# Optimization experiments

Hardware: AMD Instinct MI355X
Metric: run time of the kernel (lower is better)

## Reference

```python
import jax, jax.numpy as jnp
import numpy as np

HEAD_DIM = 64
D_MODEL = 512
B, T = 8, 2048


def setup_inputs() -> dict:
    key = jax.random.key(0)
    kx, kk, kq, kv = jax.random.split(key, 4)
    x = jax.random.normal(kx, (B, T, D_MODEL), dtype=jnp.float32)
    s = 1.0 / np.sqrt(D_MODEL)
    # torch nn.Linear weights are [out, in]
    Wk = jax.random.uniform(kk, (HEAD_DIM, D_MODEL), jnp.float32, -s, s)
    Wq = jax.random.uniform(kq, (HEAD_DIM, D_MODEL), jnp.float32, -s, s)
    Wv = jax.random.uniform(kv, (HEAD_DIM, D_MODEL), jnp.float32, -s, s)
    mask = jnp.ones((1,), dtype=bool)  # not-None sentinel -> causal masking on
    return {"x": x, "Wk": Wk, "Wq": Wq, "Wv": Wv, "mask": mask}


def reference(x, Wk, Wq, Wv, mask):
    Bc, Tc, C = x.shape
    k = jnp.einsum("btc,hc->bth", x, Wk)
    q = jnp.einsum("btc,hc->bth", x, Wq)
    v = jnp.einsum("btc,hc->bth", x, Wv)
    # NOTE: source scales by C**-0.5 where C == d_model (not head_dim)
    scores = jnp.einsum("bih,bjh->bij", q, k) * (C ** -0.5)  # [B,T,T]
    causal = jnp.tril(jnp.ones((Tc, Tc), dtype=bool))
    scores = jnp.where(causal[None, :, :], scores, -jnp.inf)
    # NOTE: source applies softmax over dim=1 (query axis), faithfully kept
    attn_weights = jax.nn.softmax(scores, axis=1)
    output = jnp.einsum("bij,bjh->bih", attn_weights, v)  # [B,T,head_dim]
    return (output, attn_weights)
```

## Files before the change

kernel.cpp:

```cpp
#include <hip/hip_runtime.h>
#include <hip/hip_bf16.h>

#define TT 2048
#define NB 8
#define DM 512
#define HD 64
static constexpr float SCALE = 0.04419417382415922f;

typedef short  s16x8 __attribute__((ext_vector_type(8)));
typedef float  f32x4 __attribute__((ext_vector_type(4)));

#define MFMA(a, b, c) __builtin_amdgcn_mfma_f32_16x16x32_bf16((a), (b), (c), 0, 0, 0)

static __device__ inline unsigned short f2bf(float f) {
    unsigned int u = __float_as_uint(f);
    u += 0x7FFFu + ((u >> 16) & 1u);
    return (unsigned short)(u >> 16);
}

__global__ __launch_bounds__(256) void prep_kernel(
    const float* __restrict__ Wk, const float* __restrict__ Wq,
    const float* __restrict__ Wv, unsigned short* __restrict__ wbf,
    float* __restrict__ colsum, float* __restrict__ out) {
    const int bi = blockIdx.x, t = threadIdx.x;
    if (bi < 256) {
        int i = (bi * 256 + t) * 4;
        *(float4*)(out + i) = make_float4(0.f, 0.f, 0.f, 0.f);
    } else if (bi < 260) {
        int i = ((bi - 256) * 256 + t) * 4;
        *(float4*)(colsum + i) = make_float4(0.f, 0.f, 0.f, 0.f);
    } else {
        int g = ((bi - 260) * 256 + t) * 4;
        int mat = g >> 15, off = g & 32767;
        const float* src = (mat == 0) ? Wk : (mat == 1) ? Wq : Wv;
        float4 f = *(const float4*)(src + off);
        wbf[g + 0] = f2bf(f.x); wbf[g + 1] = f2bf(f.y);
        wbf[g + 2] = f2bf(f.z); wbf[g + 3] = f2bf(f.w);
    }
}

__global__ __launch_bounds__(256) void rcp_kernel(float* __restrict__ p) {
    int i = (blockIdx.x * 256 + threadIdx.x) * 4;
    float4 a = *(float4*)(p + i);
    a.x = 1.0f / a.x; a.y = 1.0f / a.y; a.z = 1.0f / a.z; a.w = 1.0f / a.w;
    *(float4*)(p + i) = a;
}

#define XS 72
__global__ __launch_bounds__(256) void qkv_kernel(
    const float* __restrict__ x, const unsigned short* __restrict__ wbf,
    unsigned short* __restrict__ kb, unsigned short* __restrict__ qb,
    unsigned short* __restrict__ vb) {
    __shared__ unsigned short xs[32 * XS];
    const int i0 = blockIdx.x * 32;
    const int t = threadIdx.x;
    const int w = t >> 6, lane = t & 63;
    const int m15 = lane & 15, quad = lane >> 4;
    const int srow = t >> 3, c8 = (t & 7) * 8;
    f32x4 acc[2][3];
    for (int mt = 0; mt < 2; ++mt)
        for (int ct = 0; ct < 3; ++ct)
            acc[mt][ct] = (f32x4){0.f, 0.f, 0.f, 0.f};

    for (int kc = 0; kc < DM; kc += 64) {
        __syncthreads();
        {
            const float* gp = x + (size_t)(i0 + srow) * DM + kc + c8;
            float4 f0 = *(const float4*)gp;
            float4 f1 = *(const float4*)(gp + 4);
            s16x8 h;
            h[0] = (short)f2bf(f0.x); h[1] = (short)f2bf(f0.y);
            h[2] = (short)f2bf(f0.z); h[3] = (short)f2bf(f0.w);
            h[4] = (short)f2bf(f1.x); h[5] = (short)f2bf(f1.y);
            h[6] = (short)f2bf(f1.z); h[7] = (short)f2bf(f1.w);
            *(s16x8*)(xs + srow * XS + c8) = h;
        }
        __syncthreads();
        for (int ks = 0; ks < 2; ++ks) {
            s16x8 a[2];
            for (int mt = 0; mt < 2; ++mt)
                a[mt] = *(const s16x8*)(xs + (mt * 16 + m15) * XS + ks * 32 + quad * 8);
            for (int ct = 0; ct < 3; ++ct) {
                s16x8 bfr = *(const s16x8*)(wbf +
                    (size_t)((w * 3 + ct) * 16 + m15) * DM + kc + ks * 32 + quad * 8);
                acc[0][ct] = MFMA(a[0], bfr, acc[0][ct]);
                acc[1][ct] = MFMA(a[1], bfr, acc[1][ct]);
            }
        }
    }
    for (int mt = 0; mt < 2; ++mt)
        for (int ct = 0; ct < 3; ++ct) {
            int tile16 = w * 3 + ct;
            unsigned short* outp = (tile16 < 4) ? kb : (tile16 < 8) ? qb : vb;
            int col = (tile16 & 3) * 16 + m15;
            for (int r = 0; r < 4; ++r) {
                int grow = i0 + mt * 16 + quad * 4 + r;
                outp[(size_t)grow * HD + col] = f2bf(acc[mt][ct][r]);
            }
        }
}

__global__ __launch_bounds__(256) void colsum_kernel(
    const unsigned short* __restrict__ qb, const unsigned short* __restrict__ kb,
    float* __restrict__ colsum) {
    const int jt = blockIdx.x, ich = blockIdx.y, b = blockIdx.z;
    const int j0 = jt * 64;
    const int iend = (ich + 1) * 512;
    if (iend <= j0) return;
    const int t = threadIdx.x;
    const int w = t >> 6, lane = t & 63;
    const int m15 = lane & 15, quad = lane >> 4;
    s16x8 bk[4][2];
    for (int ct = 0; ct < 4; ++ct)
        for (int ks = 0; ks < 2; ++ks)
            bk[ct][ks] = *(const s16x8*)(kb +
                (size_t)(b * TT + j0 + ct * 16 + m15) * HD + ks * 32 + quad * 8);
    float csum[4] = {0.f, 0.f, 0.f, 0.f};
    const int istart = max(ich * 512, j0);
    for (int it = istart + w * 16; it < iend; it += 64) {
        s16x8 aq[2];
        for (int ks = 0; ks < 2; ++ks)
            aq[ks] = *(const s16x8*)(qb +
                (size_t)(b * TT + it + m15) * HD + ks * 32 + quad * 8);
        for (int ct = 0; ct < 4; ++ct) {
            f32x4 s = (f32x4){0.f, 0.f, 0.f, 0.f};
            s = MFMA(aq[0], bk[ct][0], s);
            s = MFMA(aq[1], bk[ct][1], s);
            int gj = j0 + ct * 16 + m15;
            for (int r = 0; r < 4; ++r) {
                int gi = it + quad * 4 + r;
                float e = (gj <= gi) ? __expf(s[r] * SCALE) : 0.f;
                csum[ct] += e;
            }
        }
    }
    for (int ct = 0; ct < 4; ++ct) {
        csum[ct] += __shfl_xor(csum[ct], 16);
        csum[ct] += __shfl_xor(csum[ct], 32);
    }
    if (lane < 16)
        for (int ct = 0; ct < 4; ++ct)
            atomicAdd(&colsum[b * TT + j0 + ct * 16 + lane], csum[ct]);
}

#define VS 264
#define PS 72
__global__ __launch_bounds__(256) void normpv_kernel(
    const unsigned short* __restrict__ qb, const unsigned short* __restrict__ kb,
    const unsigned short* __restrict__ vb, const float* __restrict__ rcs,
    float* __restrict__ attn, float* __restrict__ out) {
    const int jch = blockIdx.x;
    const int ti = blockIdx.y, b = blockIdx.z;
    const int i0 = ti * 64;
    const int jbase = jch * 512;
    float* abase = attn + (size_t)b * TT * TT;
    const int t = threadIdx.x;
    const float4 z = make_float4(0.f, 0.f, 0.f, 0.f);
    if (jbase > i0 + 63) {
        for (int e = 0; e < 32; ++e) {
            int f4 = e * 256 + t;
            int row = f4 >> 7, c4 = (f4 & 127) * 4;
            *(float4*)(abase + (size_t)(i0 + row) * TT + jbase + c4) = z;
        }
        return;
    }
    const int w = t >> 6, lane = t & 63;
    const int m15 = lane & 15, quad = lane >> 4;
    __shared__ unsigned short vT[64 * VS];
    __shared__ unsigned short ps[4 * 16 * PS];
    unsigned short* psw = ps + w * 16 * PS;
    s16x8 aq[2];
    for (int ks = 0; ks < 2; ++ks)
        aq[ks] = *(const s16x8*)(qb +
            (size_t)(b * TT + i0 + w * 16 + m15) * HD + ks * 32 + quad * 8);
    f32x4 o[4];
    for (int ht = 0; ht < 4; ++ht) o[ht] = (f32x4){0.f, 0.f, 0.f, 0.f};
    const float* rcb = rcs + b * TT;

    for (int half = 0; half < 2; ++half) {
        const int jh = jbase + half * 256;
        if (jh > i0 + 63) {
            for (int e = 0; e < 16; ++e) {
                int f4 = e * 256 + t;
                int row = f4 >> 6, c4 = (f4 & 63) * 4;
                *(float4*)(abase + (size_t)(i0 + row) * TT + jh + c4) = z;
            }
            continue;
        }
        __syncthreads();
        {
            const unsigned short* vp = vb + (size_t)(b * TT + jh + t) * HD;
            for (int seg = 0; seg < 8; ++seg) {
                s16x8 vv = *(const s16x8*)(vp + seg * 8);
                for (int q = 0; q < 8; ++q)
                    vT[(seg * 8 + q) * VS + t] = (unsigned short)vv[q];
            }
        }
        __syncthreads();
        for (int jt2 = 0; jt2 < 4; ++jt2) {
            const int j0 = jh + jt2 * 64;
            if (j0 > i0 + 63) {
                for (int e = 0; e < 4; ++e) {
                    int f4 = e * 256 + t;
                    int row = f4 >> 4, c4 = (f4 & 15) * 4;
                    *(float4*)(abase + (size_t)(i0 + row) * TT + j0 + c4) = z;
                }
                continue;
            }
            s16x8 bk[4][2];
            for (int ct = 0; ct < 4; ++ct)
                for (int ks = 0; ks < 2; ++ks)
                    bk[ct][ks] = *(const s16x8*)(kb +
                        (size_t)(b * TT + j0 + ct * 16 + m15) * HD + ks * 32 + quad * 8);
            for (int ct = 0; ct < 4; ++ct) {
                f32x4 s = (f32x4){0.f, 0.f, 0.f, 0.f};
                s = MFMA(aq[0], bk[ct][0], s);
                s = MFMA(aq[1], bk[ct][1], s);
                int gj = j0 + ct * 16 + m15;
                float rc = rcb[gj];
                for (int r = 0; r < 4; ++r) {
                    int gi = i0 + w * 16 + quad * 4 + r;
                    float e = (gj <= gi) ? __expf(s[r] * SCALE) : 0.f;
                    float a = e * rc;
                    abase[(size_t)gi * TT + gj] = a;
                    psw[(quad * 4 + r) * PS + ct * 16 + m15] = f2bf(a);
                }
            }
            for (int ks = 0; ks < 2; ++ks) {
                s16x8 ap = *(const s16x8*)(psw + m15 * PS + ks * 32 + quad * 8);
                for (int ht = 0; ht < 4; ++ht) {
                    s16x8 bv = *(const s16x8*)(vT +
                        (ht * 16 + m15) * VS + jt2 * 64 + ks * 32 + quad * 8);
                    o[ht] = MFMA(ap, bv, o[ht]);
                }
            }
        }
    }
    for (int ht = 0; ht < 4; ++ht)
        for (int r = 0; r < 4; ++r)
            atomicAdd(&out[(size_t)(b * TT + i0 + w * 16 + quad * 4 + r) * HD +
                           ht * 16 + m15], o[ht][r]);
}

extern "C" void kernel_launch(void* const* d_in, const int* in_sizes, int n_in,
                              void* d_out, int out_size, void* d_ws, size_t ws_size,
                              hipStream_t stream) {
    const float* x  = (const float*)d_in[0];
    const float* Wk = (const float*)d_in[1];
    const float* Wq = (const float*)d_in[2];
    const float* Wv = (const float*)d_in[3];

    float* out  = (float*)d_out;
    float* attn = out + (size_t)NB * TT * HD;

    unsigned short* kb = (unsigned short*)d_ws;
    unsigned short* qb = kb + (size_t)NB * TT * HD;
    unsigned short* vb = qb + (size_t)NB * TT * HD;
    float* colsum = (float*)(vb + (size_t)NB * TT * HD);
    unsigned short* wbf = (unsigned short*)(colsum + NB * TT);

    hipLaunchKernelGGL(prep_kernel, dim3(356), dim3(256), 0, stream,
                       Wk, Wq, Wv, wbf, colsum, out);
    hipLaunchKernelGGL(qkv_kernel,  dim3(512), dim3(256), 0, stream,
                       x, wbf, kb, qb, vb);
    hipLaunchKernelGGL(colsum_kernel, dim3(32, 4, 8), dim3(256), 0, stream,
                       qb, kb, colsum);
    hipLaunchKernelGGL(rcp_kernel,  dim3(16), dim3(256), 0, stream, colsum);
    hipLaunchKernelGGL(normpv_kernel, dim3(4, 32, 8), dim3(256), 0, stream,
                       qb, kb, vb, colsum, attn, out);
}
```

Measured before the change: 226.7 us.

## Store V transposed, drop LDS transpose and reciprocal kernel, fix zeroing ranges

The QKV projection now writes V directly in a per-batch transposed layout, so the normalize-PV kernel reads V fragments straight from global memory. This removes the shared-memory transpose and its two barriers and flattens the loop to eight 64-column tiles. The separate reciprocal kernel is gone; the reciprocal of the column sum is computed inline where it is used, saving one launch. The prep kernel now zeroes all of `out` and `colsum`, where it previously covered only a quarter of each. The transposed V stores are scattered 2-byte writes, and V is now read from global memory with a large stride instead of from shared memory.

```diff
diff --git a/kernel.cpp b/kernel.cpp
--- a/kernel.cpp
+++ b/kernel.cpp
@@ -23,14 +23,14 @@
     const float* __restrict__ Wv, unsigned short* __restrict__ wbf,
     float* __restrict__ colsum, float* __restrict__ out) {
     const int bi = blockIdx.x, t = threadIdx.x;
-    if (bi < 256) {
+    if (bi < 1024) {
         int i = (bi * 256 + t) * 4;
         *(float4*)(out + i) = make_float4(0.f, 0.f, 0.f, 0.f);
-    } else if (bi < 260) {
-        int i = ((bi - 256) * 256 + t) * 4;
+    } else if (bi < 1040) {
+        int i = ((bi - 1024) * 256 + t) * 4;
         *(float4*)(colsum + i) = make_float4(0.f, 0.f, 0.f, 0.f);
     } else {
-        int g = ((bi - 260) * 256 + t) * 4;
+        int g = ((bi - 1040) * 256 + t) * 4;
         int mat = g >> 15, off = g & 32767;
         const float* src = (mat == 0) ? Wk : (mat == 1) ? Wq : Wv;
         float4 f = *(const float4*)(src + off);
@@ -39,18 +39,11 @@
     }
 }
 
-__global__ __launch_bounds__(256) void rcp_kernel(float* __restrict__ p) {
-    int i = (blockIdx.x * 256 + threadIdx.x) * 4;
-    float4 a = *(float4*)(p + i);
-    a.x = 1.0f / a.x; a.y = 1.0f / a.y; a.z = 1.0f / a.z; a.w = 1.0f / a.w;
-    *(float4*)(p + i) = a;
-}
-
 #define XS 72
 __global__ __launch_bounds__(256) void qkv_kernel(
     const float* __restrict__ x, const unsigned short* __restrict__ wbf,
     unsigned short* __restrict__ kb, unsigned short* __restrict__ qb,
-    unsigned short* __restrict__ vb) {
+    unsigned short* __restrict__ vbT) {
     __shared__ unsigned short xs[32 * XS];
     const int i0 = blockIdx.x * 32;
     const int t = threadIdx.x;
@@ -91,11 +84,19 @@
     for (int mt = 0; mt < 2; ++mt)
         for (int ct = 0; ct < 3; ++ct) {
             int tile16 = w * 3 + ct;
-            unsigned short* outp = (tile16 < 4) ? kb : (tile16 < 8) ? qb : vb;
             int col = (tile16 & 3) * 16 + m15;
-            for (int r = 0; r < 4; ++r) {
-                int grow = i0 + mt * 16 + quad * 4 + r;
-                outp[(size_t)grow * HD + col] = f2bf(acc[mt][ct][r]);
+            if (tile16 < 8) {
+                unsigned short* outp = (tile16 < 4) ? kb : qb;
+                for (int r = 0; r < 4; ++r) {
+                    int grow = i0 + mt * 16 + quad * 4 + r;
+                    outp[(size_t)grow * HD + col] = f2bf(acc[mt][ct][r]);
+                }
+            } else {
+                for (int r = 0; r < 4; ++r) {
+                    int grow = i0 + mt * 16 + quad * 4 + r;
+                    int bb = grow >> 11, tt = grow & 2047;
+                    vbT[((size_t)bb * HD + col) * TT + tt] = f2bf(acc[mt][ct][r]);
+                }
             }
         }
 }
@@ -143,11 +144,10 @@
             atomicAdd(&colsum[b * TT + j0 + ct * 16 + lane], csum[ct]);
 }
 
-#define VS 264
 #define PS 72
 __global__ __launch_bounds__(256) void normpv_kernel(
     const unsigned short* __restrict__ qb, const unsigned short* __restrict__ kb,
-    const unsigned short* __restrict__ vb, const float* __restrict__ rcs,
+    const unsigned short* __restrict__ vbT, const float* __restrict__ colsum,
     float* __restrict__ attn, float* __restrict__ out) {
     const int jch = blockIdx.x;
     const int ti = blockIdx.y, b = blockIdx.z;
@@ -166,7 +166,6 @@
     }
     const int w = t >> 6, lane = t & 63;
     const int m15 = lane & 15, quad = lane >> 4;
-    __shared__ unsigned short vT[64 * VS];
     __shared__ unsigned short ps[4 * 16 * PS];
     unsigned short* psw = ps + w * 16 * PS;
     s16x8 aq[2];
@@ -175,64 +174,44 @@
             (size_t)(b * TT + i0 + w * 16 + m15) * HD + ks * 32 + quad * 8);
     f32x4 o[4];
     for (int ht = 0; ht < 4; ++ht) o[ht] = (f32x4){0.f, 0.f, 0.f, 0.f};
-    const float* rcb = rcs + b * TT;
-
-    for (int half = 0; half < 2; ++half) {
-        const int jh = jbase + half * 256;
-        if (jh > i0 + 63) {
-            for (int e = 0; e < 16; ++e) {
+    const float* csb = colsum + b * TT;
+    const unsigned short* vbb = vbT + (size_t)b * HD * TT;
+
+    for (int jt = 0; jt < 8; ++jt) {
+        const int j0 = jbase + jt * 64;
+        if (j0 > i0 + 63) {
+            for (int e = 0; e < 4; ++e) {
                 int f4 = e * 256 + t;
-                int row = f4 >> 6, c4 = (f4 & 63) * 4;
-                *(float4*)(abase + (size_t)(i0 + row) * TT + jh + c4) = z;
+                int row = f4 >> 4, c4 = (f4 & 15) * 4;
+                *(float4*)(abase + (size_t)(i0 + row) * TT + j0 + c4) = z;
             }
             continue;
         }
-        __syncthreads();
-        {
-            const unsigned short* vp = vb + (size_t)(b * TT + jh + t) * HD;
-            for (int seg = 0; seg < 8; ++seg) {
-                s16x8 vv = *(const s16x8*)(vp + seg * 8);
-                for (int q = 0; q < 8; ++q)
-                    vT[(seg * 8 + q) * VS + t] = (unsigned short)vv[q];
-            }
-        }
-        __syncthreads();
-        for (int jt2 = 0; jt2 < 4; ++jt2) {
-            const int j0 = jh + jt2 * 64;
-            if (j0 > i0 + 63) {
-                for (int e = 0; e < 4; ++e) {
-                    int f4 = e * 256 + t;
-                    int row = f4 >> 4, c4 = (f4 & 15) * 4;
-                    *(float4*)(abase + (size_t)(i0 + row) * TT + j0 + c4) = z;
-                }
-                continue;
-            }
-            s16x8 bk[4][2];
-            for (int ct = 0; ct < 4; ++ct)
-                for (int ks = 0; ks < 2; ++ks)
-                    bk[ct][ks] = *(const s16x8*)(kb +
-                        (size_t)(b * TT + j0 + ct * 16 + m15) * HD + ks * 32 + quad * 8);
-            for (int ct = 0; ct < 4; ++ct) {
-                f32x4 s = (f32x4){0.f, 0.f, 0.f, 0.f};
-                s = MFMA(aq[0], bk[ct][0], s);
-                s = MFMA(aq[1], bk[ct][1], s);
-                int gj = j0 + ct * 16 + m15;
-                float rc = rcb[gj];
-                for (int r = 0; r < 4; ++r) {
-                    int gi = i0 + w * 16 + quad * 4 + r;
-                    float e = (gj <= gi) ? __expf(s[r] * SCALE) : 0.f;
-                    float a = e * rc;
-                    abase[(size_t)gi * TT + gj] = a;
-                    psw[(quad * 4 + r) * PS + ct * 16 + m15] = f2bf(a);
-                }
-            }
-            for (int ks = 0; ks < 2; ++ks) {
-                s16x8 ap = *(const s16x8*)(psw + m15 * PS + ks * 32 + quad * 8);
-                for (int ht = 0; ht < 4; ++ht) {
-                    s16x8 bv = *(const s16x8*)(vT +
-                        (ht * 16 + m15) * VS + jt2 * 64 + ks * 32 + quad * 8);
-                    o[ht] = MFMA(ap, bv, o[ht]);
-                }
+        s16x8 bk[4][2];
+        for (int ct = 0; ct < 4; ++ct)
+            for (int ks = 0; ks < 2; ++ks)
+                bk[ct][ks] = *(const s16x8*)(kb +
+                    (size_t)(b * TT + j0 + ct * 16 + m15) * HD + ks * 32 + quad * 8);
+        for (int ct = 0; ct < 4; ++ct) {
+            f32x4 s = (f32x4){0.f, 0.f, 0.f, 0.f};
+            s = MFMA(aq[0], bk[ct][0], s);
+            s = MFMA(aq[1], bk[ct][1], s);
+            int gj = j0 + ct * 16 + m15;
+            float rc = 1.0f / csb[gj];
+            for (int r = 0; r < 4; ++r) {
+                int gi = i0 + w * 16 + quad * 4 + r;
+                float e = (gj <= gi) ? __expf(s[r] * SCALE) : 0.f;
+                float a = e * rc;
+                abase[(size_t)gi * TT + gj] = a;
+                psw[(quad * 4 + r) * PS + ct * 16 + m15] = f2bf(a);
+            }
+        }
+        for (int ks = 0; ks < 2; ++ks) {
+            s16x8 ap = *(const s16x8*)(psw + m15 * PS + ks * 32 + quad * 8);
+            for (int ht = 0; ht < 4; ++ht) {
+                s16x8 bv = *(const s16x8*)(vbb +
+                    (size_t)(ht * 16 + m15) * TT + j0 + ks * 32 + quad * 8);
+                o[ht] = MFMA(ap, bv, o[ht]);
             }
         }
     }
@@ -253,19 +232,18 @@
     float* out  = (float*)d_out;
     float* attn = out + (size_t)NB * TT * HD;
 
-    unsigned short* kb = (unsigned short*)d_ws;
-    unsigned short* qb = kb + (size_t)NB * TT * HD;
-    unsigned short* vb = qb + (size_t)NB * TT * HD;
-    float* colsum = (float*)(vb + (size_t)NB * TT * HD);
+    unsigned short* kb  = (unsigned short*)d_ws;
+    unsigned short* qb  = kb + (size_t)NB * TT * HD;
+    unsigned short* vbT = qb + (size_t)NB * TT * HD;
+    float* colsum = (float*)(vbT + (size_t)NB * TT * HD);
     unsigned short* wbf = (unsigned short*)(colsum + NB * TT);
 
-    hipLaunchKernelGGL(prep_kernel, dim3(356), dim3(256), 0, stream,
+    hipLaunchKernelGGL(prep_kernel, dim3(1136), dim3(256), 0, stream,
                        Wk, Wq, Wv, wbf, colsum, out);
     hipLaunchKernelGGL(qkv_kernel,  dim3(512), dim3(256), 0, stream,
-                       x, wbf, kb, qb, vb);
+                       x, wbf, kb, qb, vbT);
     hipLaunchKernelGGL(colsum_kernel, dim3(32, 4, 8), dim3(256), 0, stream,
                        qb, kb, colsum);
-    hipLaunchKernelGGL(rcp_kernel,  dim3(16), dim3(256), 0, stream, colsum);
     hipLaunchKernelGGL(normpv_kernel, dim3(4, 32, 8), dim3(256), 0, stream,
-                       qb, kb, vb, colsum, attn, out);
-}
+                       qb, kb, vbT, colsum, attn, out);
+}
```

After: 242.6 us. +7.0%, slower.
